# Kernel tuning notes

Hardware: AMD Instinct MI355X
Metric: run time of the kernel (lower is better)

## Reference

```python
import jax, jax.numpy as jnp
import numpy as np

H = 1024
B = 8
S = 2048

def setup_inputs() -> dict:
    key = jax.random.key(0)
    ks = jax.random.split(key, 16)
    w = lambda k, shp: (jax.random.normal(k, shp, dtype=jnp.float32) * 0.02)
    return {
        "hidden_states": jax.random.normal(ks[0], (B, S, H), dtype=jnp.float32),
        "context_vector": jax.random.normal(ks[1], (B, H), dtype=jnp.float32),
        # nn.Linear weights stored torch-style as [out, in]
        "Wq": w(ks[2], (H, H)), "bq": w(ks[3], (H,)),
        "Wk": w(ks[4], (H, H)), "bk": w(ks[5], (H,)),
        "Wv": w(ks[6], (H, H)), "bv": w(ks[7], (H,)),
        "Wcq": w(ks[8], (H, H)),  # only .weight.t() used in original (no bias)
        "Wck": w(ks[9], (H, H)),
        "g_qh": jax.random.normal(ks[10], (H, 1), dtype=jnp.float32),
        "g_kh": jax.random.normal(ks[11], (H, 1), dtype=jnp.float32),
        "g_qc": jax.random.normal(ks[12], (H, 1), dtype=jnp.float32),
        "g_kc": jax.random.normal(ks[13], (H, 1), dtype=jnp.float32),
    }

def reference(hidden_states, context_vector, Wq, bq, Wk, bk, Wv, bv, Wcq, Wck, g_qh, g_kh, g_qc, g_kc):
    # Linear projections (torch Linear: x @ W.T + b)
    query = jnp.einsum('bsh,oh->bso', hidden_states, Wq) + bq   # [B,S,H]
    key_  = jnp.einsum('bsh,oh->bso', hidden_states, Wk) + bk
    value = jnp.einsum('bsh,oh->bso', hidden_states, Wv) + bv

    # gate = sigmoid(Q @ g_h + (ctx @ g_c)[:,None,:])  -> [B,S,1]
    q_gate = jax.nn.sigmoid(query @ g_qh + (context_vector @ g_qc)[:, None, :])
    k_gate = jax.nn.sigmoid(key_  @ g_kh + (context_vector @ g_kc)[:, None, :])

    # context projections: ctx @ weight.t() (no bias in original usage) -> [B,1,H]
    ctx_q = (context_vector @ Wcq.T)[:, None, :]
    ctx_k = (context_vector @ Wck.T)[:, None, :]

    query_hat = (1.0 - q_gate) * query + q_gate * ctx_q
    key_hat   = (1.0 - k_gate) * key_  + k_gate * ctx_k

    scale = 1.0 / jnp.sqrt(jnp.asarray(H, dtype=jnp.float32))
    scores = jnp.einsum('bqh,bkh->bqk', query_hat, key_hat) * scale  # [B,S,S]
    probs = jax.nn.softmax(scores, axis=-1)
    output = jnp.einsum('bqk,bkh->bqh', probs, value)  # [B,S,H]
    return (output, scores)
```

## Files before the change

### kernel.cpp

```cpp
#include <hip/hip_runtime.h>
#include <cstdint>
#include <cstddef>

#define H 1024
#define NB 8
#define S 2048
#define MROWS (NB*S)

using short8 = __attribute__((ext_vector_type(8))) short;
using f32x4  = __attribute__((ext_vector_type(4))) float;

__device__ __forceinline__ unsigned short f2bf(float f){
  union { float f; unsigned int u; } c; c.f = f;
  unsigned int u = c.u;
  return (unsigned short)((u + 0x7fffu + ((u >> 16) & 1u)) >> 16);
}


__global__ void k_cvt1(const float* __restrict__ src, unsigned short* __restrict__ dst){
  int i = (blockIdx.x * 256 + threadIdx.x) * 4;
  float4 v = *reinterpret_cast<const float4*>(src + i);
  ushort4 o;
  o.x = f2bf(v.x); o.y = f2bf(v.y); o.z = f2bf(v.z); o.w = f2bf(v.w);
  *reinterpret_cast<ushort4*>(dst + i) = o;
}

__global__ __launch_bounds__(256) void k_transpose(const float* __restrict__ Wq_, const float* __restrict__ Wk_,
    unsigned short* __restrict__ Wqt_, unsigned short* __restrict__ Wkt_){
  const float* src = blockIdx.z ? Wk_ : Wq_;
  unsigned short* dst = blockIdx.z ? Wkt_ : Wqt_;
  __shared__ unsigned short tl[64][65];
  const int t = threadIdx.x;
  const int bx = blockIdx.x, by = blockIdx.y;
  const int co = (t & 15) * 4;
  #pragma unroll
  for (int pass = 0; pass < 4; ++pass){
    const int ro = (t >> 4) + pass * 16;
    float4 v = *reinterpret_cast<const float4*>(src + (size_t)(by*64 + ro) * H + bx*64 + co);
    tl[co + 0][ro] = f2bf(v.x);
    tl[co + 1][ro] = f2bf(v.y);
    tl[co + 2][ro] = f2bf(v.z);
    tl[co + 3][ro] = f2bf(v.w);
  }
  __syncthreads();
  #pragma unroll
  for (int pass = 0; pass < 4; ++pass){
    const int hh = (t >> 4) + pass * 16;
    const int oo = (t & 15) * 4;
    ushort4 w;
    w.x = tl[hh][oo + 0]; w.y = tl[hh][oo + 1]; w.z = tl[hh][oo + 2]; w.w = tl[hh][oo + 3];
    *reinterpret_cast<ushort4*>(dst + (size_t)(bx*64 + hh) * H + by*64 + oo) = w;
  }
}

__global__ void k_colproj(const float* __restrict__ Wq_, const float* __restrict__ Wk_,
                          const float* __restrict__ gqh, const float* __restrict__ gkh,
                          const float* __restrict__ bq, const float* __restrict__ bk,
                          float* __restrict__ up4){
  const int z = blockIdx.z;
  const float* W = (z == 0 || z == 2) ? Wq_ : Wk_;
  const float* g = (z == 0) ? gqh : (z == 1) ? gkh : (z == 2) ? bk : bq;
  const int in = blockIdx.x * 256 + threadIdx.x;
  const int o0 = blockIdx.y * 128;
  float s = 0.f;
  for (int o = 0; o < 128; ++o) s = fmaf(W[(size_t)(o0 + o) * H + in], g[o0 + o], s);
  up4[(z * 8 + blockIdx.y) * 1024 + in] = s;
}

__global__ void k_ucombine4(const float* __restrict__ up4, float* __restrict__ u4){
  int i = blockIdx.x * 256 + threadIdx.x;
  int z = i >> 10, h = i & 1023;
  float s = 0.f;
  #pragma unroll
  for (int c = 0; c < 8; ++c) s += up4[(z * 8 + c) * 1024 + h];
  u4[i] = s;
}

__global__ __launch_bounds__(256) void k_ctxproj(const float* __restrict__ Wcq, const float* __restrict__ Wck,
    const float* __restrict__ ctx, float* __restrict__ outq, float* __restrict__ outk){
  __shared__ float cs[NB * H];
  const float* W = blockIdx.y ? Wck : Wcq;
  float* out = blockIdx.y ? outk : outq;
  const int t = threadIdx.x;
  for (int i = t; i < NB * H; i += 256) cs[i] = ctx[i];
  __syncthreads();
  const int wid = t >> 6, lane = t & 63;
  const int row = blockIdx.x * 4 + wid;
  float a[NB];
  #pragma unroll
  for (int b = 0; b < NB; ++b) a[b] = 0.f;
  for (int i0 = 0; i0 < H; i0 += 64){
    const float w = W[(size_t)row * H + i0 + lane];
    #pragma unroll
    for (int b = 0; b < NB; ++b) a[b] = fmaf(w, cs[b * H + i0 + lane], a[b]);
  }
  #pragma unroll
  for (int b = 0; b < NB; ++b){
    float v = a[b];
    #pragma unroll
    for (int off = 32; off > 0; off >>= 1) v += __shfl_xor(v, off);
    if (lane == 0) out[b * H + row] = v;
  }
}

__global__ __launch_bounds__(256) void k_colproj8(const float* __restrict__ Wq_, const float* __restrict__ Wk_,
    const float* __restrict__ ctxq, const float* __restrict__ ctxk, float* __restrict__ up8){
  __shared__ float cs[NB * 128];
  const int z = blockIdx.z;
  const float* W = z ? Wk_ : Wq_;
  const float* g = z ? ctxq : ctxk;
  const int t = threadIdx.x;
  const int o0 = blockIdx.y * 128;
  for (int i = t; i < NB * 128; i += 256){
    int b = i >> 7, oo = i & 127;
    cs[i] = g[b * H + o0 + oo];
  }
  __syncthreads();
  const int h = blockIdx.x * 256 + t;
  float s[NB];
  #pragma unroll
  for (int b = 0; b < NB; ++b) s[b] = 0.f;
  for (int oo = 0; oo < 128; ++oo){
    const float w = W[(size_t)(o0 + oo) * H + h];
    #pragma unroll
    for (int b = 0; b < NB; ++b) s[b] = fmaf(w, cs[b * 128 + oo], s[b]);
  }
  #pragma unroll
  for (int b = 0; b < NB; ++b)
    up8[z * 65536 + blockIdx.y * 8192 + b * 1024 + h] = s[b];
}

__global__ void k_ucombine8(const float* __restrict__ up8, float* __restrict__ uXY){
  int i = blockIdx.x * 256 + threadIdx.x;
  int z = i >> 13, rem = i & 8191;
  float s = 0.f;
  #pragma unroll
  for (int y = 0; y < 8; ++y) s += up8[z * 65536 + y * 8192 + rem];
  uXY[i] = s;
}

__global__ __launch_bounds__(512) void k_scalars(const float* __restrict__ bq, const float* __restrict__ gqh,
    const float* __restrict__ bk, const float* __restrict__ gkh,
    const float* __restrict__ ctx, const float* __restrict__ gqc, const float* __restrict__ gkc,
    const float* __restrict__ ctxq, const float* __restrict__ ctxk, float* __restrict__ scal){
  const int wid = threadIdx.x >> 6, lane = threadIdx.x & 63;
  for (int d = wid; d < 43; d += 8){
    const float *pa, *pb;
    if (d == 0){ pa = bq; pb = gqh; }
    else if (d == 1){ pa = bk; pb = gkh; }
    else if (d < 10){ pa = ctx + (d - 2) * H; pb = gqc; }
    else if (d < 18){ pa = ctx + (d - 10) * H; pb = gkc; }
    else if (d == 18){ pa = bq; pb = bk; }
    else if (d < 27){ pa = bq; pb = ctxk + (d - 19) * H; }
    else if (d < 35){ pa = ctxq + (d - 27) * H; pb = bk; }
    else { pa = ctxq + (d - 35) * H; pb = ctxk + (d - 35) * H; }
    float s = 0.f;
    for (int i = lane; i < H; i += 64) s = fmaf(pa[i], pb[i], s);
    #pragma unroll
    for (int off = 32; off > 0; off >>= 1) s += __shfl_xor(s, off);
    if (lane == 0) scal[d] = s;
  }
}

__global__ __launch_bounds__(256) void k_prepass(const float* __restrict__ hs,
    const float* __restrict__ u4, const float* __restrict__ uXY, const float* __restrict__ scal,
    unsigned short* __restrict__ hsb, float* __restrict__ Prow, float* __restrict__ Qcol){
  const int t = threadIdx.x, wid = t >> 6, lane = t & 63;
  const int row = blockIdx.x * 4 + wid;
  const int b = row >> 11;
  const float* hrow = hs + (size_t)row * H;
  const float* u_q = u4;
  const float* u_k = u4 + 1024;
  const float* aq  = u4 + 2048;
  const float* ak  = u4 + 3072;
  const float* uXb = uXY + b * 1024;
  const float* uYb = uXY + 8192 + b * 1024;
  unsigned short* orow = hsb + (size_t)row * H;
  float d1 = 0.f, d2 = 0.f, d3 = 0.f, d4 = 0.f, d5 = 0.f, d6 = 0.f;
  #pragma unroll
  for (int c = 0; c < 4; ++c){
    const int idx = (lane + c * 64) * 4;
    float4 v  = *reinterpret_cast<const float4*>(hrow + idx);
    float4 a1 = *reinterpret_cast<const float4*>(u_q + idx);
    float4 a2 = *reinterpret_cast<const float4*>(u_k + idx);
    float4 a3 = *reinterpret_cast<const float4*>(aq + idx);
    float4 a4 = *reinterpret_cast<const float4*>(ak + idx);
    float4 a5 = *reinterpret_cast<const float4*>(uXb + idx);
    float4 a6 = *reinterpret_cast<const float4*>(uYb + idx);
    ushort4 o; o.x = f2bf(v.x); o.y = f2bf(v.y); o.z = f2bf(v.z); o.w = f2bf(v.w);
    *reinterpret_cast<ushort4*>(orow + idx) = o;
    d1 += v.x*a1.x + v.y*a1.y + v.z*a1.z + v.w*a1.w;
    d2 += v.x*a2.x + v.y*a2.y + v.z*a2.z + v.w*a2.w;
    d3 += v.x*a3.x + v.y*a3.y + v.z*a3.z + v.w*a3.w;
    d4 += v.x*a4.x + v.y*a4.y + v.z*a4.z + v.w*a4.w;
    d5 += v.x*a5.x + v.y*a5.y + v.z*a5.z + v.w*a5.w;
    d6 += v.x*a6.x + v.y*a6.y + v.z*a6.z + v.w*a6.w;
  }
  #pragma unroll
  for (int off = 32; off > 0; off >>= 1){
    d1 += __shfl_xor(d1, off); d2 += __shfl_xor(d2, off); d3 += __shfl_xor(d3, off);
    d4 += __shfl_xor(d4, off); d5 += __shfl_xor(d5, off); d6 += __shfl_xor(d6, off);
  }
  if (lane == 0){
    float gqv = 1.f / (1.f + __expf(-(d1 + scal[0] + scal[2 + b])));
    float gkv = 1.f / (1.f + __expf(-(d2 + scal[1] + scal[10 + b])));
    float X = d5 + scal[19 + b];
    float Y = d6 + scal[27 + b];
    float eq = 1.f - gqv, ek = 1.f - gkv;
    float4 P; P.x = eq; P.y = eq * (d3 + scal[18]); P.z = eq * X; P.w = gqv;
    float4 Q; Q.x = ek; Q.y = ek * d4; Q.z = gkv; Q.w = ek * Y + gkv * scal[35 + b];
    reinterpret_cast<float4*>(Prow)[row] = P;
    reinterpret_cast<float4*>(Qcol)[row] = Q;
  }
}


#define STG(bufi, opi, halfi, koff, P0, P1) \
  { __builtin_amdgcn_global_load_lds((const __attribute__((address_space(1))) void*)(P0 + (koff)), \
      (__attribute__((address_space(3))) void*)((char*)(&lds[bufi][opi][halfi][0]) + (wid*2+0)*1024), 16, 0, 0); \
    __builtin_amdgcn_global_load_lds((const __attribute__((address_space(1))) void*)(P1 + (koff)), \
      (__attribute__((address_space(3))) void*)((char*)(&lds[bufi][opi][halfi][0]) + (wid*2+1)*1024), 16, 0, 0); }
#define STG_A(bufi, halfi, koff) STG(bufi, 0, halfi, koff, sA0, sA1)
#define STG_B(bufi, halfi, koff) STG(bufi, 1, halfi, koff, sB0, sB1)

#define DS_A(bufi, ks, mh) \
  { _Pragma("unroll") for (int m_ = 0; m_ < 4; ++m_){ \
      const int ar_ = wr*128 + ((mh)*4 + m_)*16 + (lane & 15); \
      const int sl_ = (lane >> 4) ^ ((ar_ >> 1) & 3); \
      af[m_] = *reinterpret_cast<const short8*>(&lds[bufi][0][ks][ar_*32 + sl_*8]); } }
#define DS_B(bufi, ks) \
  { _Pragma("unroll") for (int n_ = 0; n_ < 4; ++n_){ \
      const int br_ = wc*64 + n_*16 + (lane & 15); \
      const int sl_ = (lane >> 4) ^ ((br_ >> 1) & 3); \
      bf[n_] = *reinterpret_cast<const short8*>(&lds[bufi][1][ks][br_*32 + sl_*8]); } }
#define MFMA16(mh) \
  { __builtin_amdgcn_s_setprio(1); \
    _Pragma("unroll") for (int m_ = 0; m_ < 4; ++m_) \
      _Pragma("unroll") for (int n_ = 0; n_ < 4; ++n_) \
        acc[(mh)*4 + m_][n_] = __builtin_amdgcn_mfma_f32_16x16x32_bf16(af[m_], bf[n_], acc[(mh)*4 + m_][n_], 0, 0, 0); \
    __builtin_amdgcn_s_setprio(0); }
#define VM4() asm volatile("s_waitcnt vmcnt(4)" ::: "memory");
#define VM0() asm volatile("s_waitcnt vmcnt(0)" ::: "memory");
#define BAR() { asm volatile("" ::: "memory"); __builtin_amdgcn_s_barrier(); asm volatile("" ::: "memory"); }

template<int MODE>
__global__ __launch_bounds__(512, 2)
void k_gemm(const unsigned short* __restrict__ A, const unsigned short* __restrict__ B,
            int K, int ldA, int ldB, long long Abatch, long long Bbatch,
            const float* __restrict__ gate, const float* __restrict__ bias,
            const float* __restrict__ ctxv,
            unsigned short* __restrict__ outb, float* __restrict__ outf,
            long long outBatch, float scale)
{
  __shared__ __align__(16) short lds[2][2][2][8192];

  const int t = threadIdx.x;
  const int wid = t >> 6, lane = t & 63;
  const int wr = wid >> 2, wc = wid & 3;
  const int bz = blockIdx.z;
  const unsigned short* Ab = A + (size_t)bz * (size_t)Abatch;
  const unsigned short* Bb = B + (size_t)bz * (size_t)Bbatch;
  const int row0 = blockIdx.x * 256;
  const int col0 = blockIdx.y * 256;

  const int c0 = (wid*2 + 0)*64 + lane;
  const int c1 = (wid*2 + 1)*64 + lane;
  const int r0s = c0 >> 2, r1s = c1 >> 2;
  const int kc0 = (c0 & 3) ^ ((r0s >> 1) & 3);
  const int kc1 = (c1 & 3) ^ ((r1s >> 1) & 3);
  const unsigned short* sA0 = Ab + (size_t)(row0 + r0s) * (size_t)ldA + kc0*8;
  const unsigned short* sA1 = Ab + (size_t)(row0 + r1s) * (size_t)ldA + kc1*8;
  const unsigned short* sB0 = Bb + (size_t)(col0 + r0s) * (size_t)ldB + kc0*8;
  const unsigned short* sB1 = Bb + (size_t)(col0 + r1s) * (size_t)ldB + kc1*8;

  f32x4 acc[8][4] = {};
  short8 af[4], bf[4];

  STG_A(0, 0, 0); STG_B(0, 0, 0); STG_A(0, 1, 32); STG_B(0, 1, 32);
  VM0(); BAR();

  const int niter = K >> 7;
  for (int it = 0; it < niter; ++it){
    const int t1k = (it*2 + 1) << 6;
    const int t2k = (it*2 + 2) << 6;
    const bool more = (it + 1 < niter);
    DS_A(0, 0, 0); DS_B(0, 0); STG_A(1, 0, t1k); MFMA16(0); BAR();
    DS_A(0, 0, 1); STG_B(1, 0, t1k); MFMA16(1); VM4(); BAR();
    DS_A(0, 1, 0); DS_B(0, 1); STG_A(1, 1, t1k + 32); MFMA16(0); BAR();
    DS_A(0, 1, 1); STG_B(1, 1, t1k + 32); MFMA16(1);
    if (more) { VM4(); } else { VM0(); }
    BAR();
    DS_A(1, 0, 0); DS_B(1, 0); if (more) STG_A(0, 0, t2k); MFMA16(0); BAR();
    DS_A(1, 0, 1); if (more) { STG_B(0, 0, t2k); } MFMA16(1); if (more) VM4(); BAR();
    DS_A(1, 1, 0); DS_B(1, 1); if (more) STG_A(0, 1, t2k + 32); MFMA16(0); BAR();
    DS_A(1, 1, 1); if (more) { STG_B(0, 1, t2k + 32); } MFMA16(1); if (more) VM4(); BAR();
  }

  if constexpr (MODE == 0){
    #pragma unroll
    for (int mi = 0; mi < 8; ++mi)
      #pragma unroll
      for (int n = 0; n < 4; ++n)
        #pragma unroll
        for (int r = 0; r < 4; ++r){
          const int grow = row0 + wr*128 + mi*16 + (lane >> 4)*4 + r;
          const int gcol = col0 + wc*64 + n*16 + (lane & 15);
          outb[(size_t)grow * H + gcol] = f2bf(acc[mi][n][r]);
        }
  } else if constexpr (MODE == 2){
    short* tp = (short*)lds;
    const int bb = row0 >> 11;
    const int s0 = row0 & (S - 1);
    #pragma unroll
    for (int ci = 0; ci < 2; ++ci)
      #pragma unroll
      for (int cj = 0; cj < 2; ++cj){
        __syncthreads();
        if (wr == ci && (wc >> 1) == cj){
          const int lc0 = (wc & 1) * 64;
          #pragma unroll
          for (int mi = 0; mi < 8; ++mi)
            #pragma unroll
            for (int n = 0; n < 4; ++n)
              #pragma unroll
              for (int r = 0; r < 4; ++r){
                const int lr = mi*16 + (lane >> 4)*4 + r;
                const int lc = lc0 + n*16 + (lane & 15);
                tp[lr*129 + lc] = (short)f2bf(acc[mi][n][r] + bias[col0 + cj*128 + lc]);
              }
        }
        __syncthreads();
        const int hl = t >> 2;
        const int sb = (t & 3) * 32;
        unsigned short* vout = outb + (size_t)bb * H * S + (size_t)(col0 + cj*128 + hl) * S
                                    + (size_t)(s0 + ci*128 + sb);
        #pragma unroll
        for (int i2 = 0; i2 < 32; i2 += 4){
          ushort4 o;
          o.x = (unsigned short)tp[(sb + i2 + 0)*129 + hl];
          o.y = (unsigned short)tp[(sb + i2 + 1)*129 + hl];
          o.z = (unsigned short)tp[(sb + i2 + 2)*129 + hl];
          o.w = (unsigned short)tp[(sb + i2 + 3)*129 + hl];
          *reinterpret_cast<ushort4*>(vout + i2) = o;
        }
      }
  } else if constexpr (MODE == 3){
    float* PQ = (float*)lds;
    __syncthreads();
    if (t < 256){
      float4 p = reinterpret_cast<const float4*>(gate)[(size_t)bz * S + row0 + t];
      PQ[t] = p.x; PQ[256 + t] = p.y; PQ[512 + t] = p.z; PQ[768 + t] = p.w;
    } else if (t < 512){
      const int j = t - 256;
      float4 q = reinterpret_cast<const float4*>(ctxv)[(size_t)bz * S + col0 + j];
      PQ[1024 + j] = q.x; PQ[1280 + j] = q.y; PQ[1536 + j] = q.z; PQ[1792 + j] = q.w;
    }
    __syncthreads();
    float q1[4], q2[4], q3[4], q4[4];
    #pragma unroll
    for (int n = 0; n < 4; ++n){
      const int lc = wc*64 + n*16 + (lane & 15);
      q1[n] = PQ[1024 + lc]; q2[n] = PQ[1280 + lc]; q3[n] = PQ[1536 + lc]; q4[n] = PQ[1792 + lc];
    }
    #pragma unroll
    for (int mi = 0; mi < 8; ++mi)
      #pragma unroll
      for (int r = 0; r < 4; ++r){
        const int lr = wr*128 + mi*16 + (lane >> 4)*4 + r;
        const float p1 = PQ[lr], p2 = PQ[256 + lr], p3 = PQ[512 + lr], p4 = PQ[768 + lr];
        #pragma unroll
        for (int n = 0; n < 4; ++n){
          const int gcol = col0 + wc*64 + n*16 + (lane & 15);
          const float g = acc[mi][n][r];
          const float val = q1[n] * fmaf(p1, g, p2) + p1 * q2[n] + p3 * q3[n] + p4 * q4[n];
          outf[(size_t)bz * (size_t)outBatch + (size_t)(row0 + lr) * S + gcol] = scale * val;
        }
      }
  } else {
    #pragma unroll
    for (int mi = 0; mi < 8; ++mi)
      #pragma unroll
      for (int n = 0; n < 4; ++n)
        #pragma unroll
        for (int r = 0; r < 4; ++r){
          const int grow = row0 + wr*128 + mi*16 + (lane >> 4)*4 + r;
          const int gcol = col0 + wc*64 + n*16 + (lane & 15);
          outf[(size_t)bz * (size_t)outBatch + (size_t)grow * H + gcol] = acc[mi][n][r];
        }
  }
}

__global__ void k_mreduce(const float* __restrict__ mpart, unsigned short* __restrict__ Mt){
  const int i4 = (blockIdx.x * 256 + threadIdx.x) * 4;
  float4 s = *reinterpret_cast<const float4*>(mpart + i4);
  #pragma unroll
  for (int kz = 1; kz < 4; ++kz){
    float4 p = *reinterpret_cast<const float4*>(mpart + (size_t)kz * 1048576 + i4);
    s.x += p.x; s.y += p.y; s.z += p.z; s.w += p.w;
  }
  ushort4 o; o.x = f2bf(s.x); o.y = f2bf(s.y); o.z = f2bf(s.z); o.w = f2bf(s.w);
  *reinterpret_cast<ushort4*>(Mt + i4) = o;
}

__global__ __launch_bounds__(256) void k_softmax(const float* __restrict__ scores,
                                                 unsigned short* __restrict__ probs){
  const int row = blockIdx.x;
  const float* srow = scores + (size_t)row * S;
  unsigned short* prow = probs + (size_t)row * S;
  const int t = threadIdx.x, wid = t >> 6, lane = t & 63;
  __shared__ float red[8];
  float4 v0 = *reinterpret_cast<const float4*>(srow + t * 4);
  float4 v1 = *reinterpret_cast<const float4*>(srow + 1024 + t * 4);
  float m = fmaxf(fmaxf(fmaxf(v0.x, v0.y), fmaxf(v0.z, v0.w)),
                  fmaxf(fmaxf(v1.x, v1.y), fmaxf(v1.z, v1.w)));
  #pragma unroll
  for (int off = 32; off > 0; off >>= 1) m = fmaxf(m, __shfl_xor(m, off));
  if (lane == 0) red[wid] = m;
  __syncthreads();
  m = fmaxf(fmaxf(red[0], red[1]), fmaxf(red[2], red[3]));
  float4 e0, e1;
  e0.x = __expf(v0.x - m); e0.y = __expf(v0.y - m); e0.z = __expf(v0.z - m); e0.w = __expf(v0.w - m);
  e1.x = __expf(v1.x - m); e1.y = __expf(v1.y - m); e1.z = __expf(v1.z - m); e1.w = __expf(v1.w - m);
  float s = (e0.x + e0.y + e0.z + e0.w) + (e1.x + e1.y + e1.z + e1.w);
  #pragma unroll
  for (int off = 32; off > 0; off >>= 1) s += __shfl_xor(s, off);
  if (lane == 0) red[4 + wid] = s;
  __syncthreads();
  s = (red[4] + red[5]) + (red[6] + red[7]);
  const float inv = 1.f / s;
  ushort4 o;
  o.x = f2bf(e0.x * inv); o.y = f2bf(e0.y * inv); o.z = f2bf(e0.z * inv); o.w = f2bf(e0.w * inv);
  *reinterpret_cast<ushort4*>(prow + t * 4) = o;
  o.x = f2bf(e1.x * inv); o.y = f2bf(e1.y * inv); o.z = f2bf(e1.z * inv); o.w = f2bf(e1.w * inv);
  *reinterpret_cast<ushort4*>(prow + 1024 + t * 4) = o;
}

extern "C" void kernel_launch(void* const* d_in, const int* in_sizes, int n_in,
                              void* d_out, int out_size, void* d_ws, size_t ws_size,
                              hipStream_t stream) {
  const float* hs  = (const float*)d_in[0];
  const float* ctx = (const float*)d_in[1];
  const float* Wq  = (const float*)d_in[2];
  const float* bq  = (const float*)d_in[3];
  const float* Wk  = (const float*)d_in[4];
  const float* bk  = (const float*)d_in[5];
  const float* Wv  = (const float*)d_in[6];
  const float* bv  = (const float*)d_in[7];
  const float* Wcq = (const float*)d_in[8];
  const float* Wck = (const float*)d_in[9];
  const float* gqh = (const float*)d_in[10];
  const float* gkh = (const float*)d_in[11];
  const float* gqc = (const float*)d_in[12];
  const float* gkc = (const float*)d_in[13];

  char* ws = (char*)d_ws;
  unsigned short* hsb  = (unsigned short*)(ws);
  unsigned short* Tb   = (unsigned short*)(ws + 33554432);
  unsigned short* vt   = (unsigned short*)(ws + 67108864);
  unsigned short* wvb  = (unsigned short*)(ws + 100663296);
  unsigned short* wqt  = (unsigned short*)(ws + 102760448);
  unsigned short* wkt  = (unsigned short*)(ws + 104857600);
  unsigned short* mt   = (unsigned short*)(ws + 106954752);
  float* mpart = (float*)(ws + 109051904);
  float* up4   = (float*)(ws + 125829120);
  float* u4    = (float*)(ws + 125960192);
  float* up8   = (float*)(ws + 125976576);
  float* uXY   = (float*)(ws + 126500864);
  float* ctxq  = (float*)(ws + 126566400);
  float* ctxk  = (float*)(ws + 126599168);
  float* scal  = (float*)(ws + 126631936);
  float* Prow  = (float*)(ws + 126632192);
  float* Qcol  = (float*)(ws + 126894336);
  unsigned short* probs = (unsigned short*)ws;

  float* out_attn   = (float*)d_out;
  float* out_scores = out_attn + (size_t)MROWS * H;

  k_transpose<<<dim3(16, 16, 2), 256, 0, stream>>>(Wq, Wk, wqt, wkt);
  k_cvt1<<<1024, 256, 0, stream>>>(Wv, wvb);
  k_ctxproj<<<dim3(256, 2), 256, 0, stream>>>(Wcq, Wck, ctx, ctxq, ctxk);
  k_colproj<<<dim3(4, 8, 4), 256, 0, stream>>>(Wq, Wk, gqh, gkh, bq, bk, up4);
  k_ucombine4<<<16, 256, 0, stream>>>(up4, u4);
  k_colproj8<<<dim3(4, 8, 2), 256, 0, stream>>>(Wq, Wk, ctxq, ctxk, up8);
  k_ucombine8<<<64, 256, 0, stream>>>(up8, uXY);
  k_scalars<<<1, 512, 0, stream>>>(bq, gqh, bk, gkh, ctx, gqc, gkc, ctxq, ctxk, scal);
  k_prepass<<<MROWS / 4, 256, 0, stream>>>(hs, u4, uXY, scal, hsb, Prow, Qcol);

  k_gemm<4><<<dim3(4, 4, 4), 512, 0, stream>>>(wkt, wqt, 256, 1024, 1024, 256, 256,
      nullptr, nullptr, nullptr, nullptr, mpart, 1048576LL, 1.f);
  k_mreduce<<<1024, 256, 0, stream>>>(mpart, mt);

  k_gemm<0><<<dim3(64, 4, 1), 512, 0, stream>>>(hsb, mt, 1024, 1024, 1024, 0, 0,
      nullptr, nullptr, nullptr, Tb, nullptr, 0, 1.f);

  k_gemm<2><<<dim3(64, 4, 1), 512, 0, stream>>>(hsb, wvb, 1024, 1024, 1024, 0, 0,
      nullptr, bv, nullptr, vt, nullptr, 0, 1.f);

  k_gemm<3><<<dim3(8, 8, 8), 512, 0, stream>>>(Tb, hsb, 1024, 1024, 1024,
      (long long)S * H, (long long)S * H, Prow, nullptr, Qcol,
      nullptr, out_scores, (long long)S * S, 0.03125f);

  k_softmax<<<MROWS, 256, 0, stream>>>(out_scores, probs);

  k_gemm<4><<<dim3(8, 4, 8), 512, 0, stream>>>(probs, vt, 2048, 2048, 2048,
      (long long)S * S, (long long)H * S, nullptr, nullptr, nullptr,
      nullptr, out_attn, (long long)S * H, 1.f);
}
```

Baseline: 365.0 us.

## Add barrier/lgkm waits in GEMM loop and vectorize epilogue stores via LDS staging

The main GEMM loop now inserts an extra barrier and an explicit lgkmcnt(0) wait with a sched_barrier before each MFMA group, which constrains the compiler's scheduling of LDS reads against MFMAs. The MODE 0 epilogue stages bf16 results through LDS so each thread writes 16-byte vectors instead of scattered 2-byte stores. The MODE 2 transposed V epilogue changes its LDS layout so the readback is contiguous ushort8 loads and 16-byte global stores. The extra barriers add synchronization per k-step, while the epilogues aim to cut store transaction count.

```diff
diff --git a/kernel.cpp b/kernel.cpp
--- a/kernel.cpp
+++ b/kernel.cpp
@@ -7,8 +7,9 @@
 #define S 2048
 #define MROWS (NB*S)
 
-using short8 = __attribute__((ext_vector_type(8))) short;
-using f32x4  = __attribute__((ext_vector_type(4))) float;
+using short8  = __attribute__((ext_vector_type(8))) short;
+using ushort8 = __attribute__((ext_vector_type(8))) unsigned short;
+using f32x4   = __attribute__((ext_vector_type(4))) float;
 
 __device__ __forceinline__ unsigned short f2bf(float f){
   union { float f; unsigned int u; } c; c.f = f;
@@ -216,32 +217,33 @@
 
 
 #define STG(bufi, opi, halfi, koff, P0, P1) \
-  { __builtin_amdgcn_global_load_lds((const __attribute__((address_space(1))) void*)(P0 + (koff)), \
+  do { __builtin_amdgcn_global_load_lds((const __attribute__((address_space(1))) void*)(P0 + (koff)), \
       (__attribute__((address_space(3))) void*)((char*)(&lds[bufi][opi][halfi][0]) + (wid*2+0)*1024), 16, 0, 0); \
     __builtin_amdgcn_global_load_lds((const __attribute__((address_space(1))) void*)(P1 + (koff)), \
-      (__attribute__((address_space(3))) void*)((char*)(&lds[bufi][opi][halfi][0]) + (wid*2+1)*1024), 16, 0, 0); }
+      (__attribute__((address_space(3))) void*)((char*)(&lds[bufi][opi][halfi][0]) + (wid*2+1)*1024), 16, 0, 0); } while(0)
 #define STG_A(bufi, halfi, koff) STG(bufi, 0, halfi, koff, sA0, sA1)
 #define STG_B(bufi, halfi, koff) STG(bufi, 1, halfi, koff, sB0, sB1)
 
 #define DS_A(bufi, ks, mh) \
-  { _Pragma("unroll") for (int m_ = 0; m_ < 4; ++m_){ \
+  do { _Pragma("unroll") for (int m_ = 0; m_ < 4; ++m_){ \
       const int ar_ = wr*128 + ((mh)*4 + m_)*16 + (lane & 15); \
       const int sl_ = (lane >> 4) ^ ((ar_ >> 1) & 3); \
-      af[m_] = *reinterpret_cast<const short8*>(&lds[bufi][0][ks][ar_*32 + sl_*8]); } }
+      af[m_] = *reinterpret_cast<const short8*>(&lds[bufi][0][ks][ar_*32 + sl_*8]); } } while(0)
 #define DS_B(bufi, ks) \
-  { _Pragma("unroll") for (int n_ = 0; n_ < 4; ++n_){ \
+  do { _Pragma("unroll") for (int n_ = 0; n_ < 4; ++n_){ \
       const int br_ = wc*64 + n_*16 + (lane & 15); \
       const int sl_ = (lane >> 4) ^ ((br_ >> 1) & 3); \
-      bf[n_] = *reinterpret_cast<const short8*>(&lds[bufi][1][ks][br_*32 + sl_*8]); } }
+      bf[n_] = *reinterpret_cast<const short8*>(&lds[bufi][1][ks][br_*32 + sl_*8]); } } while(0)
 #define MFMA16(mh) \
-  { __builtin_amdgcn_s_setprio(1); \
+  do { __builtin_amdgcn_s_setprio(1); \
     _Pragma("unroll") for (int m_ = 0; m_ < 4; ++m_) \
       _Pragma("unroll") for (int n_ = 0; n_ < 4; ++n_) \
         acc[(mh)*4 + m_][n_] = __builtin_amdgcn_mfma_f32_16x16x32_bf16(af[m_], bf[n_], acc[(mh)*4 + m_][n_], 0, 0, 0); \
-    __builtin_amdgcn_s_setprio(0); }
-#define VM4() asm volatile("s_waitcnt vmcnt(4)" ::: "memory");
-#define VM0() asm volatile("s_waitcnt vmcnt(0)" ::: "memory");
-#define BAR() { asm volatile("" ::: "memory"); __builtin_amdgcn_s_barrier(); asm volatile("" ::: "memory"); }
+    __builtin_amdgcn_s_setprio(0); } while(0)
+#define VM4() do { asm volatile("s_waitcnt vmcnt(4)" ::: "memory"); } while(0)
+#define VM0() do { asm volatile("s_waitcnt vmcnt(0)" ::: "memory"); } while(0)
+#define BAR() do { asm volatile("" ::: "memory"); __builtin_amdgcn_s_barrier(); asm volatile("" ::: "memory"); } while(0)
+#define LGKM0() do { asm volatile("s_waitcnt lgkmcnt(0)" ::: "memory"); __builtin_amdgcn_sched_barrier(0); } while(0)
 
 template<int MODE>
 __global__ __launch_bounds__(512, 2)
@@ -284,31 +286,44 @@
     const int t1k = (it*2 + 1) << 6;
     const int t2k = (it*2 + 2) << 6;
     const bool more = (it + 1 < niter);
-    DS_A(0, 0, 0); DS_B(0, 0); STG_A(1, 0, t1k); MFMA16(0); BAR();
-    DS_A(0, 0, 1); STG_B(1, 0, t1k); MFMA16(1); VM4(); BAR();
-    DS_A(0, 1, 0); DS_B(0, 1); STG_A(1, 1, t1k + 32); MFMA16(0); BAR();
-    DS_A(0, 1, 1); STG_B(1, 1, t1k + 32); MFMA16(1);
-    if (more) { VM4(); } else { VM0(); }
-    BAR();
-    DS_A(1, 0, 0); DS_B(1, 0); if (more) STG_A(0, 0, t2k); MFMA16(0); BAR();
-    DS_A(1, 0, 1); if (more) { STG_B(0, 0, t2k); } MFMA16(1); if (more) VM4(); BAR();
-    DS_A(1, 1, 0); DS_B(1, 1); if (more) STG_A(0, 1, t2k + 32); MFMA16(0); BAR();
-    DS_A(1, 1, 1); if (more) { STG_B(0, 1, t2k + 32); } MFMA16(1); if (more) VM4(); BAR();
+    DS_A(0, 0, 0); DS_B(0, 0); STG_A(1, 0, t1k);      BAR(); LGKM0(); MFMA16(0);                              BAR();
+    DS_A(0, 0, 1);             STG_B(1, 0, t1k);      BAR(); LGKM0(); MFMA16(1); VM4();                       BAR();
+    DS_A(0, 1, 0); DS_B(0, 1); STG_A(1, 1, t1k + 32); BAR(); LGKM0(); MFMA16(0);                              BAR();
+    DS_A(0, 1, 1);             STG_B(1, 1, t1k + 32); BAR(); LGKM0(); MFMA16(1); if (more) { VM4(); } else { VM0(); } BAR();
+    DS_A(1, 0, 0); DS_B(1, 0); if (more) { STG_A(0, 0, t2k); }      BAR(); LGKM0(); MFMA16(0);                BAR();
+    DS_A(1, 0, 1);             if (more) { STG_B(0, 0, t2k); }      BAR(); LGKM0(); MFMA16(1); if (more) { VM4(); } BAR();
+    DS_A(1, 1, 0); DS_B(1, 1); if (more) { STG_A(0, 1, t2k + 32); } BAR(); LGKM0(); MFMA16(0);                BAR();
+    DS_A(1, 1, 1);             if (more) { STG_B(0, 1, t2k + 32); } BAR(); LGKM0(); MFMA16(1); if (more) { VM4(); } BAR();
   }
 
   if constexpr (MODE == 0){
-    #pragma unroll
-    for (int mi = 0; mi < 8; ++mi)
+    unsigned short* tp = (unsigned short*)lds;
+    #pragma unroll
+    for (int ci = 0; ci < 2; ++ci){
+      __syncthreads();
+      if (wr == ci){
+        #pragma unroll
+        for (int mi = 0; mi < 8; ++mi)
+          #pragma unroll
+          for (int n = 0; n < 4; ++n)
+            #pragma unroll
+            for (int r = 0; r < 4; ++r){
+              const int lr = mi*16 + (lane >> 4)*4 + r;
+              const int lc = wc*64 + n*16 + (lane & 15);
+              tp[lr*264 + lc] = f2bf(acc[mi][n][r]);
+            }
+      }
+      __syncthreads();
+      const int rr = t & 127;
+      const int cc = (t >> 7) * 64;
+      const unsigned short* srcp = tp + rr*264 + cc;
+      unsigned short* dst = outb + (size_t)(row0 + ci*128 + rr) * H + col0 + cc;
       #pragma unroll
-      for (int n = 0; n < 4; ++n)
-        #pragma unroll
-        for (int r = 0; r < 4; ++r){
-          const int grow = row0 + wr*128 + mi*16 + (lane >> 4)*4 + r;
-          const int gcol = col0 + wc*64 + n*16 + (lane & 15);
-          outb[(size_t)grow * H + gcol] = f2bf(acc[mi][n][r]);
-        }
+      for (int i = 0; i < 64; i += 8)
+        *reinterpret_cast<ushort8*>(dst + i) = *reinterpret_cast<const ushort8*>(srcp + i);
+    }
   } else if constexpr (MODE == 2){
-    short* tp = (short*)lds;
+    unsigned short* tp = (unsigned short*)lds;
     const int bb = row0 >> 11;
     const int s0 = row0 & (S - 1);
     #pragma unroll
@@ -326,23 +341,18 @@
               for (int r = 0; r < 4; ++r){
                 const int lr = mi*16 + (lane >> 4)*4 + r;
                 const int lc = lc0 + n*16 + (lane & 15);
-                tp[lr*129 + lc] = (short)f2bf(acc[mi][n][r] + bias[col0 + cj*128 + lc]);
+                tp[lc*136 + lr] = f2bf(acc[mi][n][r] + bias[col0 + cj*128 + lc]);
               }
         }
         __syncthreads();
-        const int hl = t >> 2;
-        const int sb = (t & 3) * 32;
-        unsigned short* vout = outb + (size_t)bb * H * S + (size_t)(col0 + cj*128 + hl) * S
-                                    + (size_t)(s0 + ci*128 + sb);
+        const int hh = t & 127;
+        const int sc = (t >> 7) * 32;
+        const unsigned short* srcp = tp + hh*136 + sc;
+        unsigned short* vout = outb + (size_t)bb * H * S + (size_t)(col0 + cj*128 + hh) * S
+                                    + (size_t)(s0 + ci*128 + sc);
         #pragma unroll
-        for (int i2 = 0; i2 < 32; i2 += 4){
-          ushort4 o;
-          o.x = (unsigned short)tp[(sb + i2 + 0)*129 + hl];
-          o.y = (unsigned short)tp[(sb + i2 + 1)*129 + hl];
-          o.z = (unsigned short)tp[(sb + i2 + 2)*129 + hl];
-          o.w = (unsigned short)tp[(sb + i2 + 3)*129 + hl];
-          *reinterpret_cast<ushort4*>(vout + i2) = o;
-        }
+        for (int i2 = 0; i2 < 32; i2 += 8)
+          *reinterpret_cast<ushort8*>(vout + i2) = *reinterpret_cast<const ushort8*>(srcp + i2);
       }
   } else if constexpr (MODE == 3){
     float* PQ = (float*)lds;
```

Result: no change. 367.2 us (+0.6%).
